# Performance work log

Measured on AMD Instinct MI355X. Metric: run time of the kernel, lower is better.

The kernel has to match this reference:

```python
import jax, jax.numpy as jnp
import numpy as np

B, N, H, F, G = 16, 192, 128, 128, 50


def setup_inputs() -> dict:
    key = jax.random.key(0)
    ks = jax.random.split(key, 12)
    s = lambda fan_in: 1.0 / np.sqrt(fan_in)
    inp = {
        "features": jax.random.normal(ks[0], (B, N, H), jnp.float32),
        "rbf": jax.random.uniform(ks[1], (B, N, N, G), jnp.float32),
        "neighbour_mask": jax.random.randint(ks[2], (B, N, N), 0, 2, jnp.int32),
        # dense_rbf: Linear(G,F) -> Softplus -> Linear(F,F)
        "W_rbf1": jax.random.uniform(ks[3], (G, F), jnp.float32, -s(G), s(G)),
        "b_rbf1": jnp.zeros((F,), jnp.float32),
        "W_rbf2": jax.random.uniform(ks[4], (F, F), jnp.float32, -s(F), s(F)),
        "b_rbf2": jnp.zeros((F,), jnp.float32),
        # dense_f: Linear(H,F)
        "W_f": jax.random.uniform(ks[5], (H, F), jnp.float32, -s(H), s(H)),
        "b_f": jnp.zeros((F,), jnp.float32),
        # dense_out: Linear(F,H) -> Softplus -> Linear(H,H)
        "W_o1": jax.random.uniform(ks[6], (F, H), jnp.float32, -s(F), s(F)),
        "b_o1": jnp.zeros((H,), jnp.float32),
        "W_o2": jax.random.uniform(ks[7], (H, H), jnp.float32, -s(H), s(H)),
        "b_o2": jnp.zeros((H,), jnp.float32),
    }
    return inp


def reference(features, rbf, neighbour_mask, W_rbf1, b_rbf1, W_rbf2, b_rbf2,
              W_f, b_f, W_o1, b_o1, W_o2, b_o2):
    # filter network on RBF expansion: [B,N,N,G] -> [B,N,N,F]
    fw = jax.nn.softplus(rbf @ W_rbf1 + b_rbf1) @ W_rbf2 + b_rbf2
    # neighbor features: [B,N,H] -> [B,1,N,F] (broadcast over central-atom axis)
    nf = (features @ W_f + b_f)[:, None, :, :]
    mask = neighbour_mask.astype(fw.dtype)[..., None]  # [B,N,N,1]
    # messages [B,N,N,F], masked sum over neighbor axis -> [B,N,F]
    aggregated = jnp.sum(fw * nf * mask, axis=2)
    out = jax.nn.softplus(aggregated @ W_o1 + b_o1) @ W_o2 + b_o2  # [B,N,H]
    return features + out
```

## Files before the change

kernel.cpp:

```cpp
#include <hip/hip_runtime.h>
#include <hip/hip_bf16.h>


typedef __bf16 bf16_t;
typedef __bf16 bf16x8 __attribute__((ext_vector_type(8)));
typedef float  f32x4  __attribute__((ext_vector_type(4)));
typedef unsigned int uintx4 __attribute__((ext_vector_type(4)));

constexpr int kB = 16, kN = 192, kH = 128, kF = 128, kG = 50;
constexpr int kRows = kB * kN;
constexpr int kOutPitch = 136;

__device__ __forceinline__ float ldf(const void* p, int i, bool bfm) {
  return bfm ? (float)((const bf16_t*)p)[i] : ((const float*)p)[i];
}

__device__ __forceinline__ float softplus_f(float x) {
  float t = __logf(1.f + __expf(fminf(x, 20.f)));
  return x > 20.f ? x : t;
}

__global__ __launch_bounds__(256) void detect_kernel(const unsigned int* __restrict__ rbf_w,
                                                     int* __restrict__ flag) {
  __shared__ int c_hi, c_zero;
  const int t = threadIdx.x;
  if (t == 0) { c_hi = 0; c_zero = 0; }
  __syncthreads();
  unsigned int w = rbf_w[(size_t)t * 40003u];
  unsigned int lo = w & 0xFFFFu;
  if (((lo >> 7) & 0xFFu) >= 128u) atomicAdd(&c_hi, 1);
  if (lo == 0u) atomicAdd(&c_zero, 1);
  __syncthreads();
  if (t == 0) *flag = (c_hi == 0 && c_zero < 200) ? 1 : 0;
}

__global__ __launch_bounds__(256) void prep_kernel(
    const void* __restrict__ W1, const void* __restrict__ W2,
    const void* __restrict__ Wf, const void* __restrict__ Wo1,
    const void* __restrict__ Wo2, const int* __restrict__ flag,
    bf16_t* __restrict__ w1t, bf16_t* __restrict__ w2t,
    bf16_t* __restrict__ wft, bf16_t* __restrict__ wo1t,
    bf16_t* __restrict__ wo2t) {
  const bool bfm = *flag != 0;
  int idx = blockIdx.x * 256 + threadIdx.x;
  if (idx < 8192) {
    int n = idx >> 6, k = idx & 63;
    w1t[idx] = (k < kG) ? (bf16_t)ldf(W1, k * kF + n, bfm) : (bf16_t)0.f;
  } else if (idx < 8192 + 16384) {
    int i2 = idx - 8192; int n = i2 >> 7, k = i2 & 127;
    w2t[i2] = (bf16_t)ldf(W2, k * kF + n, bfm);
  } else if (idx < 8192 + 2 * 16384) {
    int i2 = idx - 8192 - 16384; int n = i2 >> 7, k = i2 & 127;
    wft[i2] = (bf16_t)ldf(Wf, k * kF + n, bfm);
  } else if (idx < 8192 + 3 * 16384) {
    int i2 = idx - 8192 - 2 * 16384; int n = i2 >> 7, k = i2 & 127;
    wo1t[i2] = (bf16_t)ldf(Wo1, k * kH + n, bfm);
  } else if (idx < 8192 + 4 * 16384) {
    int i2 = idx - 8192 - 3 * 16384; int n = i2 >> 7, k = i2 & 127;
    wo2t[i2] = (bf16_t)ldf(Wo2, k * kH + n, bfm);
  }
}

__global__ __launch_bounds__(128) void nf_kernel(const void* __restrict__ features,
                                                 const bf16_t* __restrict__ wft,
                                                 const void* __restrict__ bfv,
                                                 const int* __restrict__ flag,
                                                 float* __restrict__ nf) {
  const bool bfm = *flag != 0;
  const int t = threadIdx.x, wave = t >> 6, lane = t & 63;
  const int n16 = lane & 15, q = lane >> 4;
  const int rbase = blockIdx.x * 32 + wave * 16;
  const int arow = rbase + n16;

  f32x4 acc[8];
#pragma unroll
  for (int nt = 0; nt < 8; ++nt)
#pragma unroll
    for (int r = 0; r < 4; ++r) acc[nt][r] = 0.f;

  if (bfm) {
    const bf16_t* fp = (const bf16_t*)features + (size_t)arow * kH;
#pragma unroll
    for (int ks = 0; ks < 4; ++ks) {
      bf16x8 afr = *(const bf16x8*)(fp + ks * 32 + q * 8);
#pragma unroll
      for (int nt = 0; nt < 8; ++nt) {
        bf16x8 bfr = *(const bf16x8*)(wft + (nt * 16 + n16) * kH + ks * 32 + q * 8);
        acc[nt] = __builtin_amdgcn_mfma_f32_16x16x32_bf16(afr, bfr, acc[nt], 0, 0, 0);
      }
    }
  } else {
    const float* fp = (const float*)features + (size_t)arow * kH;
#pragma unroll
    for (int ks = 0; ks < 4; ++ks) {
      f32x4 x0 = *(const f32x4*)(fp + ks * 32 + q * 8);
      f32x4 x1 = *(const f32x4*)(fp + ks * 32 + q * 8 + 4);
      bf16x8 ahi, alo;
#pragma unroll
      for (int e = 0; e < 4; ++e) {
        bf16_t h0 = (bf16_t)x0[e]; ahi[e]     = h0; alo[e]     = (bf16_t)(x0[e] - (float)h0);
        bf16_t h1 = (bf16_t)x1[e]; ahi[e + 4] = h1; alo[e + 4] = (bf16_t)(x1[e] - (float)h1);
      }
#pragma unroll
      for (int nt = 0; nt < 8; ++nt) {
        bf16x8 bfr = *(const bf16x8*)(wft + (nt * 16 + n16) * kH + ks * 32 + q * 8);
        acc[nt] = __builtin_amdgcn_mfma_f32_16x16x32_bf16(ahi, bfr, acc[nt], 0, 0, 0);
        acc[nt] = __builtin_amdgcn_mfma_f32_16x16x32_bf16(alo, bfr, acc[nt], 0, 0, 0);
      }
    }
  }
#pragma unroll
  for (int nt = 0; nt < 8; ++nt) {
    const int col = nt * 16 + n16;
    const float bv = ldf(bfv, col, bfm);
#pragma unroll
    for (int r = 0; r < 4; ++r)
      nf[(size_t)(rbase + q * 4 + r) * kF + col] = acc[nt][r] + bv;
  }
}

__global__ __launch_bounds__(256, 3) void main_kernel(
    const void* __restrict__ rbf, const int* __restrict__ nmask,
    const void* __restrict__ b1p, const void* __restrict__ b2p,
    const bf16_t* __restrict__ w1t, const bf16_t* __restrict__ w2t,
    const float* __restrict__ nf, const int* __restrict__ flag,
    float* __restrict__ agg) {
  __shared__ bf16_t s_hs[kN * 128];
  __shared__ int    s_rows[kN];
  __shared__ float  s_agg[kF];
  __shared__ int    s_cnt;

  const bool bfm = *flag != 0;
  const int bi = blockIdx.x;
  const int b  = bi / kN;
  const int t  = threadIdx.x;
  const int wave = t >> 6, lane = t & 63;
  const int n16 = lane & 15, q = lane >> 4;

  if (t == 0) s_cnt = 0;
  if (t < kF) s_agg[t] = 0.f;
  __syncthreads();
  for (int j = t; j < kN; j += 256)
    if (nmask[bi * kN + j] != 0) s_rows[atomicAdd(&s_cnt, 1)] = j;
  __syncthreads();
  const int nm = s_cnt;
  const int ntiles = (nm + 15) >> 4;
  for (int p2 = nm + t; p2 < ntiles * 16; p2 += 256) s_rows[p2] = 0;
  __syncthreads();

  float b1r[8], b2r[8];
#pragma unroll
  for (int nt = 0; nt < 8; ++nt) {
    b1r[nt] = ldf(b1p, nt * 16 + n16, bfm);
    b2r[nt] = ldf(b2p, nt * 16 + n16, bfm);
  }

  char* hsb = (char*)s_hs;

  for (int tt = wave; tt < ntiles; tt += 4) {
    const int j = s_rows[tt * 16 + n16];
    bf16x8 a0, a1;
    if (bfm) {
      const unsigned int* rp = (const unsigned int*)rbf + (size_t)bi * 4800 + j * 25;
      uintx4 u0, u1;
#pragma unroll
      for (int i = 0; i < 4; ++i) u0[i] = rp[q * 4 + i];
#pragma unroll
      for (int i = 0; i < 4; ++i) {
        const int d = 16 + q * 4 + i;
        u1[i] = (d < 25) ? rp[d] : 0u;
      }
      a0 = __builtin_bit_cast(bf16x8, u0);
      a1 = __builtin_bit_cast(bf16x8, u1);
    } else {
      const float* rp = (const float*)rbf + (size_t)bi * (kN * kG) + j * kG;
#pragma unroll
      for (int i = 0; i < 8; ++i) a0[i] = (bf16_t)rp[q * 8 + i];
#pragma unroll
      for (int i = 0; i < 8; ++i) {
        const int k1 = 32 + q * 8 + i;
        a1[i] = (bf16_t)((k1 < kG) ? rp[k1] : 0.f);
      }
    }

    f32x4 acc1[8];
#pragma unroll
    for (int nt = 0; nt < 8; ++nt)
#pragma unroll
      for (int r = 0; r < 4; ++r) acc1[nt][r] = 0.f;

#pragma unroll
    for (int nt = 0; nt < 8; ++nt) {
      bf16x8 bf0 = *(const bf16x8*)(w1t + (nt * 16 + n16) * 64 + q * 8);
      acc1[nt] = __builtin_amdgcn_mfma_f32_16x16x32_bf16(a0, bf0, acc1[nt], 0, 0, 0);
    }
#pragma unroll
    for (int nt = 0; nt < 8; ++nt) {
      bf16x8 bf1 = *(const bf16x8*)(w1t + (nt * 16 + n16) * 64 + 32 + q * 8);
      acc1[nt] = __builtin_amdgcn_mfma_f32_16x16x32_bf16(a1, bf1, acc1[nt], 0, 0, 0);
    }

#pragma unroll
    for (int nt = 0; nt < 8; ++nt) {
      const int colb = (nt * 16 + n16) * 2;
#pragma unroll
      for (int r = 0; r < 4; ++r) {
        const int row = tt * 16 + q * 4 + r;
        *(bf16_t*)(hsb + ((row * 256 + colb) ^ ((row & 7) << 4))) =
            (bf16_t)softplus_f(acc1[nt][r] + b1r[nt]);
      }
    }
  }
  __syncthreads();

  for (int tt = wave; tt < ntiles; tt += 4) {
    f32x4 acc2[8];
#pragma unroll
    for (int nt = 0; nt < 8; ++nt)
#pragma unroll
      for (int r = 0; r < 4; ++r) acc2[nt][r] = 0.f;

#pragma unroll
    for (int ks = 0; ks < 4; ++ks) {
      const int row = tt * 16 + n16;
      bf16x8 afr = *(const bf16x8*)(hsb +
          ((row * 256 + (ks * 32 + q * 8) * 2) ^ ((row & 7) << 4)));
#pragma unroll
      for (int nt = 0; nt < 8; ++nt) {
        bf16x8 bfr = *(const bf16x8*)(w2t + (nt * 16 + n16) * 128 + ks * 32 + q * 8);
        acc2[nt] = __builtin_amdgcn_mfma_f32_16x16x32_bf16(afr, bfr, acc2[nt], 0, 0, 0);
      }
    }

    const int i0 = tt * 16 + q * 4;
    int jr[4]; float wr[4];
#pragma unroll
    for (int r = 0; r < 4; ++r) {
      const int idx = i0 + r;
      jr[r] = s_rows[idx];
      wr[r] = (idx < nm) ? 1.f : 0.f;
    }
    const float* nfb = nf + (size_t)b * kN * kF;
#pragma unroll
    for (int nt = 0; nt < 8; ++nt) {
      const int f = nt * 16 + n16;
      float p = 0.f;
#pragma unroll
      for (int r = 0; r < 4; ++r)
        p = fmaf(wr[r] * (acc2[nt][r] + b2r[nt]), nfb[jr[r] * kF + f], p);
      atomicAdd(&s_agg[f], p);
    }
  }
  __syncthreads();
  if (t < kF) agg[(size_t)bi * kF + t] = s_agg[t];
}

__global__ __launch_bounds__(128) void out_kernel(
    const float* __restrict__ agg, const void* __restrict__ features,
    const bf16_t* __restrict__ wo1t, const bf16_t* __restrict__ wo2t,
    const void* __restrict__ bo1, const void* __restrict__ bo2,
    const int* __restrict__ flag, void* __restrict__ out) {
  __shared__ bf16_t s_t[32 * kOutPitch];
  const bool bfm = *flag != 0;
  const int t = threadIdx.x, wave = t >> 6, lane = t & 63;
  const int n16 = lane & 15, q = lane >> 4;
  const int rb = blockIdx.x * 32 + wave * 16;

  f32x4 acc[8];
#pragma unroll
  for (int nt = 0; nt < 8; ++nt)
#pragma unroll
    for (int r = 0; r < 4; ++r) acc[nt][r] = 0.f;

  const float* ap = agg + (size_t)(rb + n16) * kF;
#pragma unroll
  for (int ks = 0; ks < 4; ++ks) {
    f32x4 x0 = *(const f32x4*)(ap + ks * 32 + q * 8);
    f32x4 x1 = *(const f32x4*)(ap + ks * 32 + q * 8 + 4);
    bf16x8 ahi, alo;
#pragma unroll
    for (int e = 0; e < 4; ++e) {
      bf16_t h0 = (bf16_t)x0[e]; ahi[e]     = h0; alo[e]     = (bf16_t)(x0[e] - (float)h0);
      bf16_t h1 = (bf16_t)x1[e]; ahi[e + 4] = h1; alo[e + 4] = (bf16_t)(x1[e] - (float)h1);
    }
#pragma unroll
    for (int nt = 0; nt < 8; ++nt) {
      bf16x8 bfr = *(const bf16x8*)(wo1t + (nt * 16 + n16) * kF + ks * 32 + q * 8);
      acc[nt] = __builtin_amdgcn_mfma_f32_16x16x32_bf16(ahi, bfr, acc[nt], 0, 0, 0);
      acc[nt] = __builtin_amdgcn_mfma_f32_16x16x32_bf16(alo, bfr, acc[nt], 0, 0, 0);
    }
  }
#pragma unroll
  for (int nt = 0; nt < 8; ++nt) {
    const int col = nt * 16 + n16;
    const float bv = ldf(bo1, col, bfm);
#pragma unroll
    for (int r = 0; r < 4; ++r)
      s_t[(wave * 16 + q * 4 + r) * kOutPitch + col] = (bf16_t)softplus_f(acc[nt][r] + bv);
  }
  __syncthreads();

#pragma unroll
  for (int nt = 0; nt < 8; ++nt)
#pragma unroll
    for (int r = 0; r < 4; ++r) acc[nt][r] = 0.f;
#pragma unroll
  for (int ks = 0; ks < 4; ++ks) {
    bf16x8 afr = *(const bf16x8*)(s_t + (wave * 16 + n16) * kOutPitch + ks * 32 + q * 8);
#pragma unroll
    for (int nt = 0; nt < 8; ++nt) {
      bf16x8 bfr = *(const bf16x8*)(wo2t + (nt * 16 + n16) * kH + ks * 32 + q * 8);
      acc[nt] = __builtin_amdgcn_mfma_f32_16x16x32_bf16(afr, bfr, acc[nt], 0, 0, 0);
    }
  }
#pragma unroll
  for (int nt = 0; nt < 8; ++nt) {
    const int col = nt * 16 + n16;
    const float bv = ldf(bo2, col, bfm);
#pragma unroll
    for (int r = 0; r < 4; ++r) {
      const int row = rb + q * 4 + r;
      float res = ldf(features, (size_t)row * kH + col, bfm) + acc[nt][r] + bv;
      if (bfm) ((bf16_t*)out)[(size_t)row * kH + col] = (bf16_t)res;
      else     ((float*)out)[(size_t)row * kH + col]  = res;
    }
  }
}

extern "C" void kernel_launch(void* const* d_in, const int* in_sizes, int n_in,
                              void* d_out, int out_size, void* d_ws, size_t ws_size,
                              hipStream_t stream) {
  const void* features = d_in[0];
  const void* rbf      = d_in[1];
  const int*  nmask    = (const int*)d_in[2];
  const void* W1  = d_in[3];
  const void* b1  = d_in[4];
  const void* W2  = d_in[5];
  const void* b2  = d_in[6];
  const void* Wf  = d_in[7];
  const void* bfv = d_in[8];
  const void* Wo1 = d_in[9];
  const void* bo1 = d_in[10];
  const void* Wo2 = d_in[11];
  const void* bo2 = d_in[12];

  char* ws = (char*)d_ws;
  float*  nf   = (float*)ws;
  float*  agg  = (float*)(ws + 1572864);
  bf16_t* w1t  = (bf16_t*)(ws + 3145728);
  bf16_t* w2t  = (bf16_t*)(ws + 3162112);
  bf16_t* wft  = (bf16_t*)(ws + 3194880);
  bf16_t* wo1t = (bf16_t*)(ws + 3227648);
  bf16_t* wo2t = (bf16_t*)(ws + 3260416);
  int*    flag = (int*)(ws + 3293184);

  detect_kernel<<<1, 256, 0, stream>>>((const unsigned int*)rbf, flag);
  prep_kernel<<<288, 256, 0, stream>>>(W1, W2, Wf, Wo1, Wo2, flag, w1t, w2t, wft, wo1t, wo2t);
  nf_kernel<<<96, 128, 0, stream>>>(features, wft, bfv, flag, nf);
  main_kernel<<<kRows, 256, 0, stream>>>(rbf, nmask, b1, b2, w1t, w2t, nf, flag, agg);
  out_kernel<<<96, 128, 0, stream>>>(agg, features, wo1t, wo2t, bo1, bo2, flag, d_out);
}
```

Baseline: 371.9 us.

## Restructure main kernel: ballot compaction, staged RBF, per-wave fused filter MLP

```diff
diff --git a/kernel.cpp b/kernel.cpp
--- a/kernel.cpp
+++ b/kernel.cpp
@@ -5,7 +5,6 @@
 typedef __bf16 bf16_t;
 typedef __bf16 bf16x8 __attribute__((ext_vector_type(8)));
 typedef float  f32x4  __attribute__((ext_vector_type(4)));
-typedef unsigned int uintx4 __attribute__((ext_vector_type(4)));
 
 constexpr int kB = 16, kN = 192, kH = 128, kF = 128, kG = 50;
 constexpr int kRows = kB * kN;
@@ -119,33 +118,51 @@
   }
 }
 
-__global__ __launch_bounds__(256, 3) void main_kernel(
+__global__ __launch_bounds__(256) void main_kernel(
     const void* __restrict__ rbf, const int* __restrict__ nmask,
     const void* __restrict__ b1p, const void* __restrict__ b2p,
     const bf16_t* __restrict__ w1t, const bf16_t* __restrict__ w2t,
     const float* __restrict__ nf, const int* __restrict__ flag,
     float* __restrict__ agg) {
-  __shared__ bf16_t s_hs[kN * 128];
+  __shared__ __attribute__((aligned(16))) bf16_t s_a[kN * 64];
+  __shared__ __attribute__((aligned(16))) bf16_t s_t[4][16 * 128];
   __shared__ int    s_rows[kN];
-  __shared__ float  s_agg[kF];
-  __shared__ int    s_cnt;
+  __shared__ float  s_red[4][kF];
+  __shared__ int    s_bcnt[4];
 
   const bool bfm = *flag != 0;
   const int bi = blockIdx.x;
   const int b  = bi / kN;
   const int t  = threadIdx.x;
-  const int wave = t >> 6, lane = t & 63;
+  const int wv = t >> 6, lane = t & 63;
   const int n16 = lane & 15, q = lane >> 4;
 
-  if (t == 0) s_cnt = 0;
-  if (t < kF) s_agg[t] = 0.f;
-  __syncthreads();
-  for (int j = t; j < kN; j += 256)
-    if (nmask[bi * kN + j] != 0) s_rows[atomicAdd(&s_cnt, 1)] = j;
-  __syncthreads();
-  const int nm = s_cnt;
+  int active = (t < kN) ? (nmask[bi * kN + t] != 0 ? 1 : 0) : 0;
+  unsigned long long bal = __ballot(active != 0);
+  if (lane == 0) s_bcnt[wv] = __popcll(bal);
+  __syncthreads();
+  const int c0 = s_bcnt[0], c1 = s_bcnt[1], c2c = s_bcnt[2];
+  const int nm = c0 + c1 + c2c;
+  const int prefix = (wv > 0 ? c0 : 0) + (wv > 1 ? c1 : 0) + (wv > 2 ? c2c : 0);
+  if (active) {
+    int rank = __popcll(bal & ((1ull << lane) - 1ull));
+    s_rows[prefix + rank] = t;
+  }
   const int ntiles = (nm + 15) >> 4;
-  for (int p2 = nm + t; p2 < ntiles * 16; p2 += 256) s_rows[p2] = 0;
+  const int tot = ntiles * 16;
+  for (int idx = nm + t; idx < tot; idx += 256) s_rows[idx] = 0;
+  __syncthreads();
+
+  char* sab = (char*)s_a;
+  for (int idx = wv; idx < tot; idx += 4) {
+    const int row = s_rows[idx];
+    float v = 0.f;
+    if (lane < kG) {
+      const size_t off = ((size_t)bi * kN + row) * kG + lane;
+      v = bfm ? (float)((const bf16_t*)rbf)[off] : ((const float*)rbf)[off];
+    }
+    *(bf16_t*)(sab + ((idx * 128 + lane * 2) ^ ((idx & 7) << 4))) = (bf16_t)v;
+  }
   __syncthreads();
 
   float b1r[8], b2r[8];
@@ -155,49 +172,33 @@
     b2r[nt] = ldf(b2p, nt * 16 + n16, bfm);
   }
 
-  char* hsb = (char*)s_hs;
-
-  for (int tt = wave; tt < ntiles; tt += 4) {
-    const int j = s_rows[tt * 16 + n16];
-    bf16x8 a0, a1;
-    if (bfm) {
-      const unsigned int* rp = (const unsigned int*)rbf + (size_t)bi * 4800 + j * 25;
-      uintx4 u0, u1;
-#pragma unroll
-      for (int i = 0; i < 4; ++i) u0[i] = rp[q * 4 + i];
-#pragma unroll
-      for (int i = 0; i < 4; ++i) {
-        const int d = 16 + q * 4 + i;
-        u1[i] = (d < 25) ? rp[d] : 0u;
-      }
-      a0 = __builtin_bit_cast(bf16x8, u0);
-      a1 = __builtin_bit_cast(bf16x8, u1);
-    } else {
-      const float* rp = (const float*)rbf + (size_t)bi * (kN * kG) + j * kG;
-#pragma unroll
-      for (int i = 0; i < 8; ++i) a0[i] = (bf16_t)rp[q * 8 + i];
-#pragma unroll
-      for (int i = 0; i < 8; ++i) {
-        const int k1 = 32 + q * 8 + i;
-        a1[i] = (bf16_t)((k1 < kG) ? rp[k1] : 0.f);
-      }
-    }
-
-    f32x4 acc1[8];
+  float racc[8];
+#pragma unroll
+  for (int nt = 0; nt < 8; ++nt) racc[nt] = 0.f;
+
+  char* tb = (char*)(s_t[wv]);
+  const int swA = (n16 & 7) << 4;
+  const float* nfb = nf + (size_t)b * kN * kF;
+
+  for (int tt = wv; tt < ntiles; tt += 4) {
+    const int abase = (tt * 16 + n16) * 128;
+    bf16x8 a0 = *(const bf16x8*)(sab + ((abase + q * 16) ^ swA));
+    bf16x8 a1 = *(const bf16x8*)(sab + ((abase + 64 + q * 16) ^ swA));
+
+    f32x4 acc[8];
 #pragma unroll
     for (int nt = 0; nt < 8; ++nt)
 #pragma unroll
-      for (int r = 0; r < 4; ++r) acc1[nt][r] = 0.f;
-
-#pragma unroll
-    for (int nt = 0; nt < 8; ++nt) {
-      bf16x8 bf0 = *(const bf16x8*)(w1t + (nt * 16 + n16) * 64 + q * 8);
-      acc1[nt] = __builtin_amdgcn_mfma_f32_16x16x32_bf16(a0, bf0, acc1[nt], 0, 0, 0);
-    }
-#pragma unroll
-    for (int nt = 0; nt < 8; ++nt) {
-      bf16x8 bf1 = *(const bf16x8*)(w1t + (nt * 16 + n16) * 64 + 32 + q * 8);
-      acc1[nt] = __builtin_amdgcn_mfma_f32_16x16x32_bf16(a1, bf1, acc1[nt], 0, 0, 0);
+      for (int r = 0; r < 4; ++r) acc[nt][r] = 0.f;
+#pragma unroll
+    for (int nt = 0; nt < 8; ++nt) {
+      bf16x8 bfr = *(const bf16x8*)(w1t + (nt * 16 + n16) * 64 + q * 8);
+      acc[nt] = __builtin_amdgcn_mfma_f32_16x16x32_bf16(a0, bfr, acc[nt], 0, 0, 0);
+    }
+#pragma unroll
+    for (int nt = 0; nt < 8; ++nt) {
+      bf16x8 bfr = *(const bf16x8*)(w1t + (nt * 16 + n16) * 64 + 32 + q * 8);
+      acc[nt] = __builtin_amdgcn_mfma_f32_16x16x32_bf16(a1, bfr, acc[nt], 0, 0, 0);
     }
 
 #pragma unroll
@@ -205,30 +206,24 @@
       const int colb = (nt * 16 + n16) * 2;
 #pragma unroll
       for (int r = 0; r < 4; ++r) {
-        const int row = tt * 16 + q * 4 + r;
-        *(bf16_t*)(hsb + ((row * 256 + colb) ^ ((row & 7) << 4))) =
-            (bf16_t)softplus_f(acc1[nt][r] + b1r[nt]);
-      }
-    }
-  }
-  __syncthreads();
-
-  for (int tt = wave; tt < ntiles; tt += 4) {
-    f32x4 acc2[8];
+        const int row = q * 4 + r;
+        *(bf16_t*)(tb + ((row * 256 + colb) ^ ((row & 7) << 4))) =
+            (bf16_t)softplus_f(acc[nt][r] + b1r[nt]);
+      }
+    }
+
+    f32x4 c2[8];
 #pragma unroll
     for (int nt = 0; nt < 8; ++nt)
 #pragma unroll
-      for (int r = 0; r < 4; ++r) acc2[nt][r] = 0.f;
-
+      for (int r = 0; r < 4; ++r) c2[nt][r] = 0.f;
 #pragma unroll
     for (int ks = 0; ks < 4; ++ks) {
-      const int row = tt * 16 + n16;
-      bf16x8 afr = *(const bf16x8*)(hsb +
-          ((row * 256 + (ks * 32 + q * 8) * 2) ^ ((row & 7) << 4)));
+      bf16x8 af = *(const bf16x8*)(tb + ((n16 * 256 + ks * 64 + q * 16) ^ swA));
 #pragma unroll
       for (int nt = 0; nt < 8; ++nt) {
         bf16x8 bfr = *(const bf16x8*)(w2t + (nt * 16 + n16) * 128 + ks * 32 + q * 8);
-        acc2[nt] = __builtin_amdgcn_mfma_f32_16x16x32_bf16(afr, bfr, acc2[nt], 0, 0, 0);
+        c2[nt] = __builtin_amdgcn_mfma_f32_16x16x32_bf16(af, bfr, c2[nt], 0, 0, 0);
       }
     }
 
@@ -240,19 +235,29 @@
       jr[r] = s_rows[idx];
       wr[r] = (idx < nm) ? 1.f : 0.f;
     }
-    const float* nfb = nf + (size_t)b * kN * kF;
 #pragma unroll
     for (int nt = 0; nt < 8; ++nt) {
       const int f = nt * 16 + n16;
       float p = 0.f;
 #pragma unroll
       for (int r = 0; r < 4; ++r)
-        p = fmaf(wr[r] * (acc2[nt][r] + b2r[nt]), nfb[jr[r] * kF + f], p);
-      atomicAdd(&s_agg[f], p);
-    }
-  }
-  __syncthreads();
-  if (t < kF) agg[(size_t)bi * kF + t] = s_agg[t];
+        p = fmaf(wr[r] * (c2[nt][r] + b2r[nt]), nfb[jr[r] * kF + f], p);
+      racc[nt] += p;
+    }
+  }
+
+#pragma unroll
+  for (int nt = 0; nt < 8; ++nt) {
+    racc[nt] += __shfl_xor(racc[nt], 16);
+    racc[nt] += __shfl_xor(racc[nt], 32);
+  }
+  if (lane < 16) {
+#pragma unroll
+    for (int nt = 0; nt < 8; ++nt) s_red[wv][nt * 16 + lane] = racc[nt];
+  }
+  __syncthreads();
+  if (t < kF)
+    agg[(size_t)bi * kF + t] = s_red[0][t] + s_red[1][t] + s_red[2][t] + s_red[3][t];
 }
 
 __global__ __launch_bounds__(128) void out_kernel(
```

After: 494.9 us. +33.1%, slower.

## Process all neighbours densely with per-wave tiles and register reduction

Applied to the files above, without the earlier changes.

```diff
diff --git a/kernel.cpp b/kernel.cpp
--- a/kernel.cpp
+++ b/kernel.cpp
@@ -119,33 +119,24 @@
   }
 }
 
-__global__ __launch_bounds__(256, 3) void main_kernel(
+__global__ __launch_bounds__(256) void main_kernel(
     const void* __restrict__ rbf, const int* __restrict__ nmask,
     const void* __restrict__ b1p, const void* __restrict__ b2p,
     const bf16_t* __restrict__ w1t, const bf16_t* __restrict__ w2t,
     const float* __restrict__ nf, const int* __restrict__ flag,
     float* __restrict__ agg) {
-  __shared__ bf16_t s_hs[kN * 128];
-  __shared__ int    s_rows[kN];
-  __shared__ float  s_agg[kF];
-  __shared__ int    s_cnt;
+  __shared__ __attribute__((aligned(16))) bf16_t s_t[4][16 * 128];
+  __shared__ float s_mask[kN];
+  __shared__ float s_red[4][kF];
 
   const bool bfm = *flag != 0;
   const int bi = blockIdx.x;
   const int b  = bi / kN;
   const int t  = threadIdx.x;
-  const int wave = t >> 6, lane = t & 63;
+  const int wv = t >> 6, lane = t & 63;
   const int n16 = lane & 15, q = lane >> 4;
 
-  if (t == 0) s_cnt = 0;
-  if (t < kF) s_agg[t] = 0.f;
-  __syncthreads();
-  for (int j = t; j < kN; j += 256)
-    if (nmask[bi * kN + j] != 0) s_rows[atomicAdd(&s_cnt, 1)] = j;
-  __syncthreads();
-  const int nm = s_cnt;
-  const int ntiles = (nm + 15) >> 4;
-  for (int p2 = nm + t; p2 < ntiles * 16; p2 += 256) s_rows[p2] = 0;
+  if (t < kN) s_mask[t] = (float)nmask[bi * kN + t];
   __syncthreads();
 
   float b1r[8], b2r[8];
@@ -155,13 +146,20 @@
     b2r[nt] = ldf(b2p, nt * 16 + n16, bfm);
   }
 
-  char* hsb = (char*)s_hs;
-
-  for (int tt = wave; tt < ntiles; tt += 4) {
-    const int j = s_rows[tt * 16 + n16];
+  float racc[8];
+#pragma unroll
+  for (int nt = 0; nt < 8; ++nt) racc[nt] = 0.f;
+
+  char* tb = (char*)(s_t[wv]);
+  const int swA   = (n16 & 7) << 4;
+  const int trow0 = wv * 16;
+  const float* nfb = nf + (size_t)b * kN * kF;
+
+  for (int third = 0; third < 3; ++third) {
+    const int jrow = third * 64 + trow0 + n16;
     bf16x8 a0, a1;
     if (bfm) {
-      const unsigned int* rp = (const unsigned int*)rbf + (size_t)bi * 4800 + j * 25;
+      const unsigned int* rp = (const unsigned int*)rbf + (size_t)bi * 4800 + jrow * 25;
       uintx4 u0, u1;
 #pragma unroll
       for (int i = 0; i < 4; ++i) u0[i] = rp[q * 4 + i];
@@ -173,7 +171,7 @@
       a0 = __builtin_bit_cast(bf16x8, u0);
       a1 = __builtin_bit_cast(bf16x8, u1);
     } else {
-      const float* rp = (const float*)rbf + (size_t)bi * (kN * kG) + j * kG;
+      const float* rp = (const float*)rbf + (size_t)bi * (kN * kG) + (size_t)jrow * kG;
 #pragma unroll
       for (int i = 0; i < 8; ++i) a0[i] = (bf16_t)rp[q * 8 + i];
 #pragma unroll
@@ -188,7 +186,6 @@
     for (int nt = 0; nt < 8; ++nt)
 #pragma unroll
       for (int r = 0; r < 4; ++r) acc1[nt][r] = 0.f;
-
 #pragma unroll
     for (int nt = 0; nt < 8; ++nt) {
       bf16x8 bf0 = *(const bf16x8*)(w1t + (nt * 16 + n16) * 64 + q * 8);
@@ -205,54 +202,53 @@
       const int colb = (nt * 16 + n16) * 2;
 #pragma unroll
       for (int r = 0; r < 4; ++r) {
-        const int row = tt * 16 + q * 4 + r;
-        *(bf16_t*)(hsb + ((row * 256 + colb) ^ ((row & 7) << 4))) =
+        const int row = q * 4 + r;
+        *(bf16_t*)(tb + ((row * 256 + colb) ^ ((row & 7) << 4))) =
             (bf16_t)softplus_f(acc1[nt][r] + b1r[nt]);
       }
     }
-  }
-  __syncthreads();
-
-  for (int tt = wave; tt < ntiles; tt += 4) {
-    f32x4 acc2[8];
+
+    f32x4 c2[8];
 #pragma unroll
     for (int nt = 0; nt < 8; ++nt)
 #pragma unroll
-      for (int r = 0; r < 4; ++r) acc2[nt][r] = 0.f;
-
+      for (int r = 0; r < 4; ++r) c2[nt][r] = 0.f;
 #pragma unroll
     for (int ks = 0; ks < 4; ++ks) {
-      const int row = tt * 16 + n16;
-      bf16x8 afr = *(const bf16x8*)(hsb +
-          ((row * 256 + (ks * 32 + q * 8) * 2) ^ ((row & 7) << 4)));
+      bf16x8 af = *(const bf16x8*)(tb + ((n16 * 256 + ks * 64 + q * 16) ^ swA));
 #pragma unroll
       for (int nt = 0; nt < 8; ++nt) {
         bf16x8 bfr = *(const bf16x8*)(w2t + (nt * 16 + n16) * 128 + ks * 32 + q * 8);
-        acc2[nt] = __builtin_amdgcn_mfma_f32_16x16x32_bf16(afr, bfr, acc2[nt], 0, 0, 0);
-      }
-    }
-
-    const int i0 = tt * 16 + q * 4;
-    int jr[4]; float wr[4];
-#pragma unroll
-    for (int r = 0; r < 4; ++r) {
-      const int idx = i0 + r;
-      jr[r] = s_rows[idx];
-      wr[r] = (idx < nm) ? 1.f : 0.f;
-    }
-    const float* nfb = nf + (size_t)b * kN * kF;
+        c2[nt] = __builtin_amdgcn_mfma_f32_16x16x32_bf16(af, bfr, c2[nt], 0, 0, 0);
+      }
+    }
+
+    const int jb = third * 64 + trow0 + q * 4;
 #pragma unroll
     for (int nt = 0; nt < 8; ++nt) {
       const int f = nt * 16 + n16;
       float p = 0.f;
 #pragma unroll
-      for (int r = 0; r < 4; ++r)
-        p = fmaf(wr[r] * (acc2[nt][r] + b2r[nt]), nfb[jr[r] * kF + f], p);
-      atomicAdd(&s_agg[f], p);
-    }
-  }
-  __syncthreads();
-  if (t < kF) agg[(size_t)bi * kF + t] = s_agg[t];
+      for (int r = 0; r < 4; ++r) {
+        const int j = jb + r;
+        p = fmaf(s_mask[j] * (c2[nt][r] + b2r[nt]), nfb[(size_t)j * kF + f], p);
+      }
+      racc[nt] += p;
+    }
+  }
+
+#pragma unroll
+  for (int nt = 0; nt < 8; ++nt) {
+    racc[nt] += __shfl_xor(racc[nt], 16);
+    racc[nt] += __shfl_xor(racc[nt], 32);
+  }
+  if (lane < 16) {
+#pragma unroll
+    for (int nt = 0; nt < 8; ++nt) s_red[wv][nt * 16 + lane] = racc[nt];
+  }
+  __syncthreads();
+  if (t < kF)
+    agg[(size_t)bi * kF + t] = s_red[0][t] + s_red[1][t] + s_red[2][t] + s_red[3][t];
 }
 
 __global__ __launch_bounds__(128) void out_kernel(
```

Result: slower. 484.0 us (+30.1%).
